# Performance work log

Hardware: AMD Instinct MI355X
Metric: run time of the kernel (lower is better)

Reference implementation:

```python
import jax, jax.numpy as jnp
import numpy as np

B, S, H, NH, NL, G, D, A, T = 32, 512, 512, 8, 6, 8, 256, 18, 1024
HD = H // NH


def setup_inputs() -> dict:
    key = jax.random.key(0)
    ks = jax.random.split(key, 32)
    def n(k, shape, s=0.02):
        return jax.random.normal(k, shape, jnp.float32) * s
    return {
        'game_indices': jax.random.randint(ks[0], (B,), 0, G),
        'states': jax.random.normal(ks[1], (B, S, D), jnp.float32),
        'actions': jax.random.randint(ks[2], (B, S), 0, A),
        'returns_to_go': jax.random.normal(ks[3], (B, S), jnp.float32),
        'timesteps': jax.random.randint(ks[4], (B, S), 0, T),
        'attention_mask': jnp.ones((B, S), jnp.int32),
        'game_emb': n(ks[5], (G, H)),
        'obs_W': n(ks[6], (G, D, H)),
        'obs_b': n(ks[7], (G, H)),
        'obs_ln_g': jnp.ones((G, H), jnp.float32),
        'obs_ln_b': jnp.zeros((G, H), jnp.float32),
        'act_emb': n(ks[8], (G, A, H)),
        'ret_W': n(ks[9], (H,)),
        'ret_b': n(ks[10], (H,)),
        'time_emb': n(ks[11], (T, H)),
        'Wqkv': n(ks[12], (NL, 3 * H, H)),
        'bqkv': n(ks[13], (NL, 3 * H)),
        'Wo': n(ks[14], (NL, H, H)),
        'bo': n(ks[15], (NL, H)),
        'ln1_g': jnp.ones((NL, H), jnp.float32),
        'ln1_b': jnp.zeros((NL, H), jnp.float32),
        'W1': n(ks[16], (NL, 4 * H, H)),
        'b1': n(ks[17], (NL, 4 * H)),
        'W2': n(ks[18], (NL, H, 4 * H)),
        'b2': n(ks[19], (NL, H)),
        'ln2_g': jnp.ones((NL, H), jnp.float32),
        'ln2_b': jnp.zeros((NL, H), jnp.float32),
        'sh_W': n(ks[20], (G, H, D)),
        'sh_b': n(ks[21], (G, D)),
        'ah_W': n(ks[22], (G, H, A)),
        'ah_b': n(ks[23], (G, A)),
        'rh_W': n(ks[24], (H, 1)),
        'rh_b': n(ks[25], (1,)),
    }


def _ln(x, g, b, eps=1e-5):
    m = jnp.mean(x, -1, keepdims=True)
    v = jnp.mean((x - m) ** 2, -1, keepdims=True)
    return (x - m) / jnp.sqrt(v + eps) * g + b


def reference(game_indices, states, actions, returns_to_go, timesteps, attention_mask,
              game_emb, obs_W, obs_b, obs_ln_g, obs_ln_b, act_emb, ret_W, ret_b, time_emb,
              Wqkv, bqkv, Wo, bo, ln1_g, ln1_b, W1, b1, W2, b2, ln2_g, ln2_b,
              sh_W, sh_b, ah_W, ah_b, rh_W, rh_b):
    gi = game_indices
    g_emb = game_emb[gi][:, None, :]  # [B,1,H]
    # per-game routed observation embedding: Linear -> LayerNorm -> ReLU (grouped GEMM by game)
    se = jnp.einsum('bsd,bdh->bsh', states, obs_W[gi]) + obs_b[gi][:, None, :]
    se = jax.nn.relu(_ln(se, obs_ln_g[gi][:, None, :], obs_ln_b[gi][:, None, :]))
    # per-game routed action embedding table lookup
    ae = act_emb[gi[:, None], actions]  # [B,S,H]
    re = returns_to_go[..., None] * ret_W + ret_b  # Linear(1,H)
    te = time_emb[timesteps]
    x = se + ae + re + te + g_emb
    # key padding mask (src_key_padding_mask: True where attention_mask==0)
    bias = jnp.where((attention_mask == 0)[:, None, None, :], -1e9, 0.0)  # [B,1,1,S]
    scale = 1.0 / jnp.sqrt(jnp.asarray(HD, jnp.float32))
    for l in range(NL):  # post-norm TransformerEncoderLayer, relu, dropout=0 (eval)
        qkv = jnp.einsum('bsh,oh->bso', x, Wqkv[l]) + bqkv[l]
        q, k, v = jnp.split(qkv, 3, axis=-1)
        q = q.reshape(B, S, NH, HD).transpose(0, 2, 1, 3)
        k = k.reshape(B, S, NH, HD).transpose(0, 2, 1, 3)
        v = v.reshape(B, S, NH, HD).transpose(0, 2, 1, 3)
        scores = jnp.einsum('bhqd,bhkd->bhqk', q, k) * scale + bias
        attn = jnp.einsum('bhqk,bhkd->bhqd', jax.nn.softmax(scores, -1), v)
        attn = attn.transpose(0, 2, 1, 3).reshape(B, S, H)
        attn = jnp.einsum('bsh,oh->bso', attn, Wo[l]) + bo[l]
        x = _ln(x + attn, ln1_g[l], ln1_b[l])
        ff = jax.nn.relu(jnp.einsum('bsh,fh->bsf', x, W1[l]) + b1[l])
        ff = jnp.einsum('bsf,hf->bsh', ff, W2[l]) + b2[l]
        x = _ln(x + ff, ln2_g[l], ln2_b[l])
    # per-game routed prediction heads
    state_preds = jnp.einsum('bsh,bho->bso', x, sh_W[gi]) + sh_b[gi][:, None, :]
    action_preds = jnp.einsum('bsh,bho->bso', x, ah_W[gi]) + ah_b[gi][:, None, :]
    return_preds = x @ rh_W + rh_b
    return (state_preds, action_preds, return_preds)
```

## Files before the change

### kernel.cpp

```cpp
#include <hip/hip_runtime.h>

typedef __bf16 bf16x4 __attribute__((ext_vector_type(4)));
typedef __bf16 bf16x8 __attribute__((ext_vector_type(8)));
typedef float f32x4 __attribute__((ext_vector_type(4)));
typedef int int4v __attribute__((ext_vector_type(4)));

#define C1SM  0.18033688011112042592f

typedef const __attribute__((address_space(1))) void gvoid_t;
typedef __attribute__((address_space(3))) void lvoid_t;


__global__ void cvt_f32_bf16(const float* __restrict__ src, __bf16* __restrict__ dst, int n4)
{
    int i = blockIdx.x * blockDim.x + threadIdx.x;
    if (i >= n4) return;
    f32x4 v = *reinterpret_cast<const f32x4*>(src + (size_t)i * 4);
    bf16x4 o;
    #pragma unroll
    for (int k = 0; k < 4; ++k) o[k] = (__bf16)v[k];
    *reinterpret_cast<bf16x4*>(dst + (size_t)i * 4) = o;
}

__global__ void transpose_cvt(const float* __restrict__ src, __bf16* __restrict__ dst, int R, int C)
{
    int m = blockIdx.y;
    int n = R * C;
    int i = blockIdx.x * 256 + threadIdx.x;
    if (i >= n) return;
    int c = i / R, r = i - c * R;
    dst[(size_t)m * n + i] = (__bf16)src[(size_t)m * n + (size_t)r * C + c];
}

__global__ void transpose_f32(const float* __restrict__ src, float* __restrict__ dst, int R, int C)
{
    int m = blockIdx.y;
    int n = R * C;
    int i = blockIdx.x * 256 + threadIdx.x;
    if (i >= n) return;
    int c = i / R, r = i - c * R;
    dst[(size_t)m * n + i] = src[(size_t)m * n + (size_t)r * C + c];
}

__global__ __launch_bounds__(256, 4)
void gemm_bt(const __bf16* __restrict__ A, size_t strideA,
             const __bf16* __restrict__ B, size_t strideB,
             const float* __restrict__ bias, int strideBias,
             float* Cf, __bf16* Cb, size_t strideC,
             const int* __restrict__ gidx, int ldk, int Klen,
             size_t splitStride, int ldc, int relu, __bf16* __restrict__ vt)
{
    __shared__ __align__(16) char smem[32768];
    __bf16* lCb = (__bf16*)smem;
    float*  lCf = (float*)smem;

    const int z = blockIdx.z;
    const int g = gidx ? gidx[z] : 0;
    const __bf16* Ab = A + (splitStride ? (size_t)z * Klen : (size_t)z * strideA);
    const __bf16* Bb = B + (splitStride ? (size_t)z * Klen : (size_t)g * strideB);
    __bf16* CbO = Cb ? (Cb + (size_t)z * (splitStride ? splitStride : strideC)) : nullptr;
    float*  CfO = Cf ? (Cf + (size_t)z * strideC) : nullptr;
    const float* biasb = (bias && (!splitStride || z == 0)) ? bias + (size_t)g * strideBias : nullptr;

    const int nx = gridDim.x;
    const int nwg = nx * gridDim.y;
    int orig = blockIdx.y * nx + blockIdx.x;
    int wg = ((nwg & 7) == 0) ? ((orig & 7) * (nwg >> 3) + (orig >> 3)) : orig;
    const int bm = (wg / nx) * 128, bn = (wg % nx) * 128;

    const int t = threadIdx.x;
    const int w = t >> 6, lane = t & 63;
    const int wr = (w >> 1) * 64, wc = (w & 1) * 64;
    const int l16 = lane & 15, lk = lane >> 4;

    const int srow = lane >> 2;
    const int schunk = (lane & 3) ^ ((srow >> 1) & 3);
    const int ca = (lk ^ ((l16 >> 1) & 3)) * 8;

    f32x4 acc[4][4] = {};

    auto stage = [&](int buf, int kt) {
        __bf16* la = (__bf16*)(smem + buf * 16384);
        __bf16* lb = la + 4096;
        #pragma unroll
        for (int jj = 0; jj < 2; ++jj) {
            const __bf16* ga = Ab + (size_t)(bm + w * 32 + jj * 16 + srow) * ldk + kt + schunk * 8;
            __builtin_amdgcn_global_load_lds((gvoid_t*)ga, (lvoid_t*)&la[(w * 32 + jj * 16) * 32], 16, 0, 0);
            const __bf16* gb = Bb + (size_t)(bn + w * 32 + jj * 16 + srow) * ldk + kt + schunk * 8;
            __builtin_amdgcn_global_load_lds((gvoid_t*)gb, (lvoid_t*)&lb[(w * 32 + jj * 16) * 32], 16, 0, 0);
        }
    };

    stage(0, 0);
    __syncthreads();
    int cur = 0;
    for (int kt = 0; kt < Klen; kt += 32) {
        if (kt + 32 < Klen) stage(cur ^ 1, kt + 32);
        __bf16* la = (__bf16*)(smem + cur * 16384);
        __bf16* lb = la + 4096;
        bf16x8 af[4], bfr[4];
        #pragma unroll
        for (int i = 0; i < 4; ++i) {
            af[i]  = *reinterpret_cast<const bf16x8*>(&la[(wr + i * 16 + l16) * 32 + ca]);
            bfr[i] = *reinterpret_cast<const bf16x8*>(&lb[(wc + i * 16 + l16) * 32 + ca]);
        }
        #pragma unroll
        for (int mi = 0; mi < 4; ++mi)
            #pragma unroll
            for (int ni = 0; ni < 4; ++ni)
                acc[mi][ni] = __builtin_amdgcn_mfma_f32_16x16x32_bf16(af[mi], bfr[ni], acc[mi][ni], 0, 0, 0);
        __syncthreads();
        cur ^= 1;
    }

    if (vt && bn >= 1024) {
        const int bb = bm >> 9;
        const int s0 = (bm & 511) + wr + lk * 4;
        #pragma unroll
        for (int ni = 0; ni < 4; ++ni) {
            int c = bn + wc + ni * 16 + l16;
            float bv = biasb ? biasb[c] : 0.f;
            int hh = (c - 1024) >> 6, d = c & 63;
            __bf16* vrow = vt + ((size_t)(bb * 8 + hh) * 64 + d) * 512;
            #pragma unroll
            for (int mi = 0; mi < 4; ++mi) {
                bf16x4 o;
                #pragma unroll
                for (int j = 0; j < 4; ++j) o[j] = (__bf16)(acc[mi][ni][j] + bv);
                *reinterpret_cast<bf16x4*>(vrow + s0 + mi * 16) = o;
            }
        }
        return;
    }

    if (CbO) {
        #pragma unroll
        for (int ni = 0; ni < 4; ++ni) {
            int col = wc + ni * 16 + l16;
            float bv = biasb ? biasb[bn + col] : 0.f;
            #pragma unroll
            for (int mi = 0; mi < 4; ++mi)
                #pragma unroll
                for (int j = 0; j < 4; ++j) {
                    float v = acc[mi][ni][j] + bv;
                    if (relu) v = fmaxf(v, 0.f);
                    lCb[(wr + mi * 16 + lk * 4 + j) * 128 + col] = (__bf16)v;
                }
        }
        __syncthreads();
        #pragma unroll
        for (int it = 0; it < 8; ++it) {
            int off = it * 2048 + t * 8;
            int rl = off >> 7, col = off & 127;
            *reinterpret_cast<int4v*>(CbO + (size_t)(bm + rl) * ldc + bn + col) =
                *reinterpret_cast<const int4v*>(&lCb[off]);
        }
    } else {
        #pragma unroll
        for (int p = 0; p < 2; ++p) {
            if (p) __syncthreads();
            if (wr == p * 64) {
                #pragma unroll
                for (int ni = 0; ni < 4; ++ni) {
                    int col = wc + ni * 16 + l16;
                    float bv = biasb ? biasb[bn + col] : 0.f;
                    #pragma unroll
                    for (int mi = 0; mi < 4; ++mi)
                        #pragma unroll
                        for (int j = 0; j < 4; ++j) {
                            float v = acc[mi][ni][j] + bv;
                            if (relu) v = fmaxf(v, 0.f);
                            lCf[(mi * 16 + lk * 4 + j) * 128 + col] = v;
                        }
                }
            }
            __syncthreads();
            #pragma unroll
            for (int it = 0; it < 8; ++it) {
                int off = it * 1024 + t * 4;
                int rl = off >> 7, col = off & 127;
                *reinterpret_cast<f32x4*>(CfO + (size_t)(bm + p * 64 + rl) * ldc + bn + col) =
                    *reinterpret_cast<const f32x4*>(&lCf[off]);
            }
        }
    }
}

__global__ __launch_bounds__(256, 6)
void attn_fwd_c(const __bf16* __restrict__ qkv, const __bf16* __restrict__ vt,
                const int* __restrict__ mask, __bf16* __restrict__ out)
{
    __shared__ __bf16 lK[2][64 * 64];
    __shared__ __bf16 lV[2][64 * 64];
    __shared__ __bf16 lP[4][16 * 32];
    __shared__ float lM2[512];

    const int bh = blockIdx.x;
    const int b = bh >> 3, h = bh & 7;
    const int q0 = blockIdx.y * 128;
    const int t = threadIdx.x, w = t >> 6, lane = t & 63;
    const int l16 = lane & 15, lk = lane >> 4;

    const __bf16* qbase = qkv + (size_t)b * 512 * 1536 + h * 64;
    const __bf16* kbase = qbase + 512;
    const __bf16* vtb = vt + (size_t)(b * 8 + h) * 64 * 512;

    bf16x8 qfr[2][2];
    #pragma unroll
    for (int qn = 0; qn < 2; ++qn) {
        int row = q0 + w * 32 + qn * 16 + l16;
        #pragma unroll
        for (int kc = 0; kc < 2; ++kc)
            qfr[qn][kc] = *reinterpret_cast<const bf16x8*>(qbase + (size_t)row * 1536 + (kc * 4 + lk) * 8);
    }
    {
        int i0 = t * 2;
        lM2[i0]     = (mask[b * 512 + i0] == 0)     ? -2e9f : 0.f;
        lM2[i0 + 1] = (mask[b * 512 + i0 + 1] == 0) ? -2e9f : 0.f;
    }

    auto stageKV = [&](int buf, int kt) {
        #pragma unroll
        for (int r = 0; r < 2; ++r) {
            int c = r * 256 + w * 64 + lane;
            int row = c >> 3, ch = c & 7;
            const __bf16* ga = kbase + (size_t)(kt + row) * 1536 + ((ch ^ (row & 7)) * 8);
            __builtin_amdgcn_global_load_lds((gvoid_t*)ga,
                (lvoid_t*)(&lK[buf][0] + (r * 256 + w * 64) * 8), 16, 0, 0);
            const __bf16* gv = vtb + (size_t)row * 512 + kt + ((ch ^ (row & 7)) * 8);
            __builtin_amdgcn_global_load_lds((gvoid_t*)gv,
                (lvoid_t*)(&lV[buf][0] + (r * 256 + w * 64) * 8), 16, 0, 0);
        }
    };

    float m_run[2] = {-1e30f, -1e30f}, l_run[2] = {0.f, 0.f};
    f32x4 oacc[2][4] = {};
    const int xsw = ((l16 >> 1) & 3) << 1;

    stageKV(0, 0);
    __syncthreads();

    int cur = 0;
    for (int kt = 0; kt < 512; kt += 64) {
        if (kt + 64 < 512) stageKV(cur ^ 1, kt + 64);
        const __bf16* lKc = &lK[cur][0];
        const __bf16* lVc = &lV[cur][0];
        __bf16* lp = &lP[w][0];

        #pragma unroll
        for (int qn = 0; qn < 2; ++qn) {
            f32x4 sacc[4] = {};
            #pragma unroll
            for (int ni = 0; ni < 4; ++ni) {
                int krow = ni * 16 + l16;
                #pragma unroll
                for (int kc = 0; kc < 2; ++kc) {
                    bf16x8 kf = *reinterpret_cast<const bf16x8*>(&lKc[krow * 64 + (((kc * 4 + lk) ^ (krow & 7)) * 8)]);
                    sacc[ni] = __builtin_amdgcn_mfma_f32_16x16x32_bf16(kf, qfr[qn][kc], sacc[ni], 0, 0, 0);
                }
            }

            f32x4 mx4 = {-3e38f, -3e38f, -3e38f, -3e38f};
            #pragma unroll
            for (int ni = 0; ni < 4; ++ni) {
                f32x4 mkv = *reinterpret_cast<const f32x4*>(&lM2[kt + ni * 16 + lk * 4]);
                f32x4 sv;
                #pragma unroll
                for (int j = 0; j < 4; ++j) {
                    sv[j] = fmaf(sacc[ni][j], C1SM, mkv[j]);
                    mx4[j] = fmaxf(mx4[j], sv[j]);
                }
                sacc[ni] = sv;
            }
            float mx = fmaxf(fmaxf(mx4[0], mx4[1]), fmaxf(mx4[2], mx4[3]));
            mx = fmaxf(mx, __shfl_xor(mx, 16));
            mx = fmaxf(mx, __shfl_xor(mx, 32));
            bool need = mx > m_run[qn] + 11.54f;
            if (__any((int)need)) {
                float mn = fmaxf(m_run[qn], mx);
                float alpha = exp2f(m_run[qn] - mn);
                m_run[qn] = mn;
                l_run[qn] *= alpha;
                #pragma unroll
                for (int j = 0; j < 4; ++j) {
                    float aj = __shfl(alpha, lk * 4 + j);
                    #pragma unroll
                    for (int dn = 0; dn < 4; ++dn) oacc[qn][dn][j] *= aj;
                }
            }
            f32x4 ps4 = {0.f, 0.f, 0.f, 0.f};
            #pragma unroll
            for (int ni = 0; ni < 4; ++ni)
                #pragma unroll
                for (int j = 0; j < 4; ++j) {
                    float p = exp2f(sacc[ni][j] - m_run[qn]);
                    sacc[ni][j] = p;
                    ps4[j] += p;
                }
            l_run[qn] += (ps4[0] + ps4[1]) + (ps4[2] + ps4[3]);

            #pragma unroll
            for (int kc = 0; kc < 2; ++kc) {
                #pragma unroll
                for (int n2 = 0; n2 < 2; ++n2) {
                    bf16x4 o;
                    #pragma unroll
                    for (int j = 0; j < 4; ++j) o[j] = (__bf16)sacc[kc * 2 + n2][j];
                    *reinterpret_cast<bf16x4*>(&lp[l16 * 32 + ((n2 * 4 + lk) ^ xsw) * 4]) = o;
                }
                bf16x8 pf = *reinterpret_cast<const bf16x8*>(&lp[l16 * 32 + (lk ^ (xsw >> 1)) * 8]);
                #pragma unroll
                for (int dn = 0; dn < 4; ++dn) {
                    int vrow = dn * 16 + l16;
                    bf16x8 vf = *reinterpret_cast<const bf16x8*>(&lVc[vrow * 64 + (((kc * 4 + lk) ^ (vrow & 7)) * 8)]);
                    oacc[qn][dn] = __builtin_amdgcn_mfma_f32_16x16x32_bf16(pf, vf, oacc[qn][dn], 0, 0, 0);
                }
            }
        }
        __syncthreads();
        cur ^= 1;
    }

    #pragma unroll
    for (int qn = 0; qn < 2; ++qn) {
        float s = l_run[qn];
        s += __shfl_xor(s, 16);
        s += __shfl_xor(s, 32);
        float linv = 1.f / s;
        #pragma unroll
        for (int j = 0; j < 4; ++j) {
            float lj = __shfl(linv, lk * 4 + j);
            #pragma unroll
            for (int dn = 0; dn < 4; ++dn) {
                int row = q0 + w * 32 + qn * 16 + lk * 4 + j;
                int col = h * 64 + dn * 16 + l16;
                out[(size_t)(b * 512 + row) * 512 + col] = (__bf16)(oacc[qn][dn][j] * lj);
            }
        }
    }
}


__device__ __forceinline__ float wsum64(float v)
{
    #pragma unroll
    for (int d = 32; d >= 1; d >>= 1) v += __shfl_xor(v, d);
    return v;
}

__global__ __launch_bounds__(256)
void ln_fuse2(const __bf16* resid, const __bf16* __restrict__ pA,
              const __bf16* __restrict__ pB,
              const float* __restrict__ gamma, const float* __restrict__ beta,
              __bf16* xbo)
{
    int tok = blockIdx.x * 4 + (threadIdx.x >> 6);
    int lane = threadIdx.x & 63;
    size_t base = (size_t)tok * 512 + lane * 8;
    float y[8];
    {
        bf16x8 rv = *reinterpret_cast<const bf16x8*>(resid + base);
        bf16x8 pa = *reinterpret_cast<const bf16x8*>(pA + base);
        bf16x8 pb = *reinterpret_cast<const bf16x8*>(pB + base);
        #pragma unroll
        for (int i = 0; i < 8; ++i) y[i] = (float)rv[i] + (float)pa[i] + (float)pb[i];
    }
    float s = 0.f;
    #pragma unroll
    for (int i = 0; i < 8; ++i) s += y[i];
    float mean = wsum64(s) * (1.f / 512.f);
    float v = 0.f;
    #pragma unroll
    for (int i = 0; i < 8; ++i) { float d = y[i] - mean; v += d * d; }
    float rstd = rsqrtf(wsum64(v) * (1.f / 512.f) + 1e-5f);
    int hh = lane * 8;
    f32x4 g0 = *reinterpret_cast<const f32x4*>(gamma + hh);
    f32x4 g1 = *reinterpret_cast<const f32x4*>(gamma + hh + 4);
    f32x4 b0 = *reinterpret_cast<const f32x4*>(beta + hh);
    f32x4 b1 = *reinterpret_cast<const f32x4*>(beta + hh + 4);
    bf16x8 ob;
    #pragma unroll
    for (int i = 0; i < 4; ++i) {
        ob[i]     = (__bf16)((y[i] - mean) * rstd * g0[i] + b0[i]);
        ob[4 + i] = (__bf16)((y[4 + i] - mean) * rstd * g1[i] + b1[i]);
    }
    *reinterpret_cast<bf16x8*>(xbo + base) = ob;
}

__global__ __launch_bounds__(256)
void embed_fin(const __bf16* __restrict__ seraw, const int* __restrict__ gi,
               const int* __restrict__ actions, const float* __restrict__ rtg,
               const int* __restrict__ ts,
               const float* __restrict__ olg, const float* __restrict__ olb,
               const float* __restrict__ act_emb, const float* __restrict__ retW,
               const float* __restrict__ retb, const float* __restrict__ time_emb,
               const float* __restrict__ game_emb,
               __bf16* __restrict__ xbo)
{
    int tok = blockIdx.x * 4 + (threadIdx.x >> 6);
    int lane = threadIdx.x & 63;
    int b = tok >> 9;
    int g = gi[b];
    int a = actions[tok];
    int tt = ts[tok];
    float rv = rtg[tok];
    size_t base = (size_t)tok * 512 + lane * 8;
    int hh = lane * 8;

    float y[8];
    {
        bf16x8 a0 = *reinterpret_cast<const bf16x8*>(seraw + base);
        #pragma unroll
        for (int i = 0; i < 8; ++i) y[i] = (float)a0[i];
    }
    float s = 0.f;
    #pragma unroll
    for (int i = 0; i < 8; ++i) s += y[i];
    float mean = wsum64(s) * (1.f / 512.f);
    float v = 0.f;
    #pragma unroll
    for (int i = 0; i < 8; ++i) { float d = y[i] - mean; v += d * d; }
    float rstd = rsqrtf(wsum64(v) * (1.f / 512.f) + 1e-5f);

    const float* gp = olg + (size_t)g * 512 + hh;
    const float* bp = olb + (size_t)g * 512 + hh;
    const float* ap = act_emb + ((size_t)g * 18 + a) * 512 + hh;
    const float* tp = time_emb + (size_t)tt * 512 + hh;
    const float* ep = game_emb + (size_t)g * 512 + hh;
    const float* rwp = retW + hh;
    const float* rbp = retb + hh;

    bf16x8 ob;
    #pragma unroll
    for (int half = 0; half < 2; ++half) {
        f32x4 gv = *reinterpret_cast<const f32x4*>(gp + half * 4);
        f32x4 bv = *reinterpret_cast<const f32x4*>(bp + half * 4);
        f32x4 av = *reinterpret_cast<const f32x4*>(ap + half * 4);
        f32x4 tv = *reinterpret_cast<const f32x4*>(tp + half * 4);
        f32x4 ev = *reinterpret_cast<const f32x4*>(ep + half * 4);
        f32x4 rw = *reinterpret_cast<const f32x4*>(rwp + half * 4);
        f32x4 rb = *reinterpret_cast<const f32x4*>(rbp + half * 4);
        #pragma unroll
        for (int i = 0; i < 4; ++i) {
            float n = (y[half * 4 + i] - mean) * rstd * gv[i] + bv[i];
            n = fmaxf(n, 0.f);
            float o = n + av[i] + rv * rw[i] + rb[i] + tv[i] + ev[i];
            ob[half * 4 + i] = (__bf16)o;
        }
    }
    *reinterpret_cast<bf16x8*>(xbo + base) = ob;
}

__global__ __launch_bounds__(256)
void head_ar(const __bf16* __restrict__ xbv, const int* __restrict__ gi,
             const float* __restrict__ ahWt, const float* __restrict__ ah_b,
             const float* __restrict__ rhW, const float* __restrict__ rhb,
             float* __restrict__ outA, float* __restrict__ outR)
{
    int tok = blockIdx.x * 4 + (threadIdx.x >> 6);
    int lane = threadIdx.x & 63;
    int b = tok >> 9;
    int g = gi[b];
    size_t base = (size_t)tok * 512 + lane * 8;
    float x[8];
    {
        bf16x8 a0 = *reinterpret_cast<const bf16x8*>(xbv + base);
        #pragma unroll
        for (int i = 0; i < 8; ++i) x[i] = (float)a0[i];
    }
    #pragma unroll 1
    for (int a = 0; a < 18; ++a) {
        const float* wp = ahWt + ((size_t)g * 18 + a) * 512 + lane * 8;
        f32x4 w0 = *reinterpret_cast<const f32x4*>(wp);
        f32x4 w1 = *reinterpret_cast<const f32x4*>(wp + 4);
        float p = 0.f;
        #pragma unroll
        for (int i = 0; i < 4; ++i) { p += x[i] * w0[i]; p += x[4 + i] * w1[i]; }
        p = wsum64(p);
        if (lane == 0) outA[(size_t)tok * 18 + a] = p + ah_b[g * 18 + a];
    }
    {
        const float* wp = rhW + lane * 8;
        f32x4 w0 = *reinterpret_cast<const f32x4*>(wp);
        f32x4 w1 = *reinterpret_cast<const f32x4*>(wp + 4);
        float p = 0.f;
        #pragma unroll
        for (int i = 0; i < 4; ++i) { p += x[i] * w0[i]; p += x[4 + i] * w1[i]; }
        p = wsum64(p);
        if (lane == 0) outR[tok] = p + rhb[0];
    }
}


extern "C" void kernel_launch(void* const* d_in, const int* in_sizes, int n_in,
                              void* d_out, int out_size, void* d_ws, size_t ws_size,
                              hipStream_t stream)
{
    (void)in_sizes; (void)n_in; (void)out_size; (void)ws_size;

    const int*   gi       = (const int*)d_in[0];
    const float* states   = (const float*)d_in[1];
    const int*   actions  = (const int*)d_in[2];
    const float* rtg      = (const float*)d_in[3];
    const int*   ts       = (const int*)d_in[4];
    const int*   amask    = (const int*)d_in[5];
    const float* game_emb = (const float*)d_in[6];
    const float* obs_W    = (const float*)d_in[7];
    const float* obs_b    = (const float*)d_in[8];
    const float* obs_ln_g = (const float*)d_in[9];
    const float* obs_ln_b = (const float*)d_in[10];
    const float* act_emb  = (const float*)d_in[11];
    const float* ret_W    = (const float*)d_in[12];
    const float* ret_b    = (const float*)d_in[13];
    const float* time_emb = (const float*)d_in[14];
    const float* Wqkv     = (const float*)d_in[15];
    const float* bqkv     = (const float*)d_in[16];
    const float* Wo       = (const float*)d_in[17];
    const float* bo       = (const float*)d_in[18];
    const float* ln1_g    = (const float*)d_in[19];
    const float* ln1_b    = (const float*)d_in[20];
    const float* W1       = (const float*)d_in[21];
    const float* b1       = (const float*)d_in[22];
    const float* W2       = (const float*)d_in[23];
    const float* b2       = (const float*)d_in[24];
    const float* ln2_g    = (const float*)d_in[25];
    const float* ln2_b    = (const float*)d_in[26];
    const float* sh_W     = (const float*)d_in[27];
    const float* sh_b     = (const float*)d_in[28];
    const float* ah_W     = (const float*)d_in[29];
    const float* ah_b     = (const float*)d_in[30];
    const float* rh_W     = (const float*)d_in[31];
    const float* rh_b     = (const float*)d_in[32];

    char* wsb = (char*)d_ws;
    __bf16* tmp     = (__bf16*)(wsb + 0);
    __bf16* tmp2    = tmp + 8388608;
    __bf16* xb      = (__bf16*)(wsb + 33554432);
    __bf16* vT      = (__bf16*)(wsb + 67108864);
    __bf16* qkvB    = (__bf16*)(wsb + 83886080);
    __bf16* ff1B    = qkvB;
    __bf16* statesB = qkvB;
    __bf16* obswB   = (__bf16*)(wsb + 83886080 + 8388608);
    __bf16* attnB   = (__bf16*)(wsb + 150994944);
    __bf16* wqkvB   = (__bf16*)(wsb + 167772160);
    __bf16* woB     = (__bf16*)(wsb + 177209344);
    __bf16* w1B     = (__bf16*)(wsb + 180355072);
    __bf16* w2B     = (__bf16*)(wsb + 192937984);
    __bf16* shwB    = (__bf16*)(wsb + 205520896);
    float*  ahwT    = (float*)(wsb + 207618048);

    cvt_f32_bf16<<<4608, 256, 0, stream>>>(Wqkv, wqkvB, 1179648);
    cvt_f32_bf16<<<1536, 256, 0, stream>>>(Wo, woB, 393216);
    cvt_f32_bf16<<<6144, 256, 0, stream>>>(W1, w1B, 1572864);
    cvt_f32_bf16<<<6144, 256, 0, stream>>>(W2, w2B, 1572864);
    cvt_f32_bf16<<<4096, 256, 0, stream>>>(states, statesB, 1048576);
    transpose_cvt<<<dim3(512, 8), 256, 0, stream>>>(obs_W, obswB, 256, 512);
    transpose_cvt<<<dim3(512, 8), 256, 0, stream>>>(sh_W, shwB, 512, 256);
    transpose_f32<<<dim3(36, 8), 256, 0, stream>>>(ah_W, ahwT, 512, 18);

    gemm_bt<<<dim3(4, 4, 32), 256, 0, stream>>>(
        statesB, (size_t)512 * 256, obswB, (size_t)512 * 256, obs_b, 512,
        nullptr, tmp, (size_t)512 * 512, gi, 256, 256, 0, 512, 0, nullptr);
    embed_fin<<<4096, 256, 0, stream>>>(tmp, gi, actions, rtg, ts,
        obs_ln_g, obs_ln_b, act_emb, ret_W, ret_b, time_emb, game_emb, xb);

    for (int l = 0; l < 6; ++l) {
        gemm_bt<<<dim3(12, 128, 1), 256, 0, stream>>>(
            xb, 0, wqkvB + (size_t)l * 1536 * 512, 0, bqkv + l * 1536, 0,
            nullptr, qkvB, 0, nullptr, 512, 512, 0, 1536, 0, vT);
        attn_fwd_c<<<dim3(256, 4, 1), 256, 0, stream>>>(qkvB, vT, amask, attnB);
        gemm_bt<<<dim3(4, 128, 2), 256, 0, stream>>>(
            attnB, 0, woB + (size_t)l * 512 * 512, 0, bo + l * 512, 0,
            nullptr, tmp, 0, nullptr, 512, 256, 8388608, 512, 0, nullptr);
        ln_fuse2<<<4096, 256, 0, stream>>>(xb, tmp, tmp2, ln1_g + l * 512, ln1_b + l * 512, xb);
        gemm_bt<<<dim3(16, 128, 1), 256, 0, stream>>>(
            xb, 0, w1B + (size_t)l * 2048 * 512, 0, b1 + l * 2048, 0,
            nullptr, ff1B, 0, nullptr, 512, 512, 0, 2048, 1, nullptr);
        gemm_bt<<<dim3(4, 128, 2), 256, 0, stream>>>(
            ff1B, 0, w2B + (size_t)l * 512 * 2048, 0, b2 + l * 512, 0,
            nullptr, tmp, 0, nullptr, 2048, 1024, 8388608, 512, 0, nullptr);
        ln_fuse2<<<4096, 256, 0, stream>>>(xb, tmp, tmp2, ln2_g + l * 512, ln2_b + l * 512, xb);
    }

    gemm_bt<<<dim3(2, 4, 32), 256, 0, stream>>>(
        xb, (size_t)512 * 512, shwB, (size_t)256 * 512, sh_b, 256,
        (float*)d_out, nullptr, (size_t)512 * 256, gi, 512, 512, 0, 256, 0, nullptr);
    head_ar<<<4096, 256, 0, stream>>>(xb, gi, ahwT, ah_b, rh_W, rh_b,
        (float*)d_out + 4194304, (float*)d_out + 4489216);
}
```

Baseline: 1.425 ms.

## Add 256x256-tile GEMM kernel for the FFN up-projection

Adds a new 512-thread GEMM kernel with 256x256 output tiles, double-buffered direct-to-LDS global loads, XOR-swizzled LDS layout, MFMA scheduling in quadrants with setprio, and XCD-aware workgroup remapping. It replaces the generic gemm_bt launch for the W1 (FFN up) projection with fused bias+ReLU and a bf16 store staged through LDS. Larger tiles raise arithmetic intensity per loaded byte, at the cost of high register and LDS use (128KB LDS, two blocks per CU). The attention kernel's launch bound is also lowered from 6 to 4 waves per SIMD, which gives the compiler more registers but may reduce occupancy.

```diff
diff --git a/kernel.cpp b/kernel.cpp
--- a/kernel.cpp
+++ b/kernel.cpp
@@ -9,6 +9,10 @@
 
 typedef const __attribute__((address_space(1))) void gvoid_t;
 typedef __attribute__((address_space(3))) void lvoid_t;
+
+#define SBAR()  asm volatile("s_barrier" ::: "memory")
+#define WV0()   asm volatile("s_waitcnt vmcnt(0)" ::: "memory")
+#define WLG0()  asm volatile("s_waitcnt lgkmcnt(0)" ::: "memory")
 
 
 __global__ void cvt_f32_bf16(const float* __restrict__ src, __bf16* __restrict__ dst, int n4)
@@ -40,6 +44,129 @@
     if (i >= n) return;
     int c = i / R, r = i - c * R;
     dst[(size_t)m * n + i] = src[(size_t)m * n + (size_t)r * C + c];
+}
+
+__global__ __launch_bounds__(512, 2)
+void gemm256(const __bf16* __restrict__ A, const __bf16* __restrict__ B,
+             const float* __restrict__ bias, __bf16* __restrict__ C,
+             int ldc, int relu)
+{
+    __shared__ __bf16 lds[65536];
+
+    const int t = threadIdx.x;
+    const int w = t >> 6, lane = t & 63;
+    const int l16 = lane & 15, lk = lane >> 4;
+    const int wrl = (w >> 2) * 128;
+    const int wcl = (w & 3) * 64;
+
+    const int nx = gridDim.x;
+    const int nwg = nx * gridDim.y;
+    int orig = blockIdx.y * nx + blockIdx.x;
+    int wg = ((nwg & 7) == 0) ? ((orig & 7) * (nwg >> 3) + (orig >> 3)) : orig;
+    const int bm = (wg / nx) * 256, bn = (wg % nx) * 256;
+
+    const __bf16* Ab = A + (size_t)bm * 512;
+    const __bf16* Bb = B + (size_t)bn * 512;
+
+    f32x4 acc[8][4] = {};
+    bf16x8 af[4][2], bfr[2][2];
+
+    auto stageKt = [&](int kt) {
+        const int slot = kt & 1;
+        #pragma unroll
+        for (int h = 0; h < 4; ++h) {
+            const int m = h >> 1, hf = h & 1;
+            const __bf16* src = m ? Bb : Ab;
+            __bf16* lb = lds + slot * 32768 + m * 16384 + hf * 8192;
+            #pragma unroll
+            for (int i = 0; i < 2; ++i) {
+                int u = i * 512 + t;
+                int row = hf * 128 + (u >> 3);
+                int ch = (u & 7) ^ (row & 7);
+                const __bf16* ga = src + (size_t)row * 512 + kt * 64 + ch * 8;
+                __builtin_amdgcn_global_load_lds((gvoid_t*)ga,
+                    (lvoid_t*)(lb + (i * 512 + w * 64) * 8), 16, 0, 0);
+            }
+        }
+    };
+    auto ldA = [&](int slot, int mh) {
+        const __bf16* la = lds + slot * 32768;
+        #pragma unroll
+        for (int mi = 0; mi < 4; ++mi) {
+            int row = wrl + mh * 64 + mi * 16 + l16;
+            #pragma unroll
+            for (int ks = 0; ks < 2; ++ks) {
+                int c = (ks * 4 + lk) ^ (row & 7);
+                af[mi][ks] = *reinterpret_cast<const bf16x8*>(la + row * 64 + c * 8);
+            }
+        }
+    };
+    auto ldB = [&](int slot, int nh) {
+        const __bf16* lb = lds + slot * 32768 + 16384;
+        #pragma unroll
+        for (int nf = 0; nf < 2; ++nf) {
+            int row = wcl + nh * 32 + nf * 16 + l16;
+            #pragma unroll
+            for (int ks = 0; ks < 2; ++ks) {
+                int c = (ks * 4 + lk) ^ (row & 7);
+                bfr[nf][ks] = *reinterpret_cast<const bf16x8*>(lb + row * 64 + c * 8);
+            }
+        }
+    };
+    auto quad = [&](int mh, int nh) {
+        __builtin_amdgcn_s_setprio(1);
+        #pragma unroll
+        for (int mi = 0; mi < 4; ++mi)
+            #pragma unroll
+            for (int nf = 0; nf < 2; ++nf)
+                #pragma unroll
+                for (int ks = 0; ks < 2; ++ks)
+                    acc[mh * 4 + mi][nh * 2 + nf] = __builtin_amdgcn_mfma_f32_16x16x32_bf16(
+                        af[mi][ks], bfr[nf][ks], acc[mh * 4 + mi][nh * 2 + nf], 0, 0, 0);
+        __builtin_amdgcn_s_setprio(0);
+    };
+
+    stageKt(0);
+    #pragma unroll
+    for (int kt = 0; kt < 8; ++kt) {
+        const int slot = kt & 1;
+        WV0();
+        SBAR();
+        if (kt < 7) stageKt(kt + 1);
+        ldA(slot, 0); ldB(slot, 0);
+        SBAR(); quad(0, 0); SBAR();
+        ldB(slot, 1);
+        SBAR(); quad(0, 1); SBAR();
+        ldA(slot, 1);
+        SBAR(); quad(1, 1); SBAR();
+        ldB(slot, 0);
+        SBAR(); quad(1, 0); SBAR();
+    }
+
+    SBAR();
+    __bf16* lc = lds;
+    #pragma unroll
+    for (int nf = 0; nf < 4; ++nf) {
+        int col = wcl + nf * 16 + l16;
+        float bv = bias[bn + col];
+        #pragma unroll
+        for (int mf = 0; mf < 8; ++mf)
+            #pragma unroll
+            for (int j = 0; j < 4; ++j) {
+                float v = acc[mf][nf][j] + bv;
+                if (relu) v = fmaxf(v, 0.f);
+                lc[(wrl + mf * 16 + lk * 4 + j) * 256 + col] = (__bf16)v;
+            }
+    }
+    WLG0();
+    SBAR();
+    #pragma unroll
+    for (int i = 0; i < 16; ++i) {
+        int off = i * 4096 + t * 8;
+        int r = off >> 8, c2 = off & 255;
+        *reinterpret_cast<int4v*>(C + (size_t)(bm + r) * ldc + bn + c2) =
+            *reinterpret_cast<const int4v*>(lc + off);
+    }
 }
 
 __global__ __launch_bounds__(256, 4)
@@ -186,7 +313,7 @@
     }
 }
 
-__global__ __launch_bounds__(256, 6)
+__global__ __launch_bounds__(256, 4)
 void attn_fwd_c(const __bf16* __restrict__ qkv, const __bf16* __restrict__ vt,
                 const int* __restrict__ mask, __bf16* __restrict__ out)
 {
@@ -573,9 +700,8 @@
             attnB, 0, woB + (size_t)l * 512 * 512, 0, bo + l * 512, 0,
             nullptr, tmp, 0, nullptr, 512, 256, 8388608, 512, 0, nullptr);
         ln_fuse2<<<4096, 256, 0, stream>>>(xb, tmp, tmp2, ln1_g + l * 512, ln1_b + l * 512, xb);
-        gemm_bt<<<dim3(16, 128, 1), 256, 0, stream>>>(
-            xb, 0, w1B + (size_t)l * 2048 * 512, 0, b1 + l * 2048, 0,
-            nullptr, ff1B, 0, nullptr, 512, 512, 0, 2048, 1, nullptr);
+        gemm256<<<dim3(8, 64), 512, 0, stream>>>(
+            xb, w1B + (size_t)l * 2048 * 512, b1 + l * 2048, ff1B, 2048, 1);
         gemm_bt<<<dim3(4, 128, 2), 256, 0, stream>>>(
             ff1B, 0, w2B + (size_t)l * 512 * 2048, 0, b2 + l * 512, 0,
             nullptr, tmp, 0, nullptr, 2048, 1024, 8388608, 512, 0, nullptr);
```

New measurement: 1.387 ms (median of 2 runs). 1.03x faster.
